# Performance work log

Hardware: AMD Instinct MI355X
Metric: run time of the kernel (lower is better)

Reference implementation:

```python
import jax, jax.numpy as jnp
import numpy as np

NX, NY = 256, 256            # img_size
NUM_DET, VIEW = 368, 180
SDD, SCD = 1000.0, 500.0
DCD = SDD - SCD
DET_INT = 2.0
PX = 1.0                     # pixel_size
SHIFT = 0.0                  # no quarter offset


def _geometry():
    # Faithful numpy port of FP.param_setting (equally_spaced mode)
    d_beta = np.pi * 360.0 / VIEW / 180.0
    beta = np.linspace(0.0, (VIEW - 1) * d_beta, VIEW)
    axis_x = np.linspace(-NX / 2, NX / 2, NX + 1) * PX          # [NX+1]
    axis_y = np.linspace(-NY / 2, NY / 2, NY + 1) * PX          # [NY+1]
    range_det_x = np.ones(NUM_DET) * DCD
    range_det_y = np.linspace(-(NUM_DET - 1) / 2, (NUM_DET - 1) / 2, NUM_DET) * DET_INT + SHIFT
    src = np.array([-SCD, 0.0])
    cb, sb = np.cos(beta), np.sin(beta)
    src_point = np.stack([src[0] * cb + src[1] * sb, -src[0] * sb + src[1] * cb])  # [2, V]
    det_x_rot = cb[None, :] * range_det_x[:, None] + sb[None, :] * range_det_y[:, None]   # [D, V]
    det_y_rot = -sb[None, :] * range_det_x[:, None] + cb[None, :] * range_det_y[:, None]  # [D, V]
    ax = (axis_x[:, None] - src_point[0][None, :])[None, :, :] / (det_x_rot - src_point[0])[:, None, :]  # [D, NX+1, V]
    ay = (axis_y[:, None] - src_point[1][None, :])[None, :, :] / (det_y_rot - src_point[1])[:, None, :]  # [D, NY+1, V]
    a_min = np.maximum(np.minimum(ax[:, 0, :], ax[:, -1, :]), np.minimum(ay[:, 0, :], ay[:, -1, :]))
    a_min[a_min < 0] = 0.0
    a_max = np.minimum(np.maximum(ax[:, 0, :], ax[:, -1, :]), np.maximum(ay[:, 0, :], ay[:, -1, :]))
    a_max[a_max > 1] = 1.0
    axy = np.concatenate([ax, ay], axis=1)                       # [D, NX+NY+2, V]
    axy[(axy > a_max[:, None, :]) | (axy < a_min[:, None, :])] = np.nan
    axy = np.sort(axy, axis=1)                                   # NaNs sort to the end (matches torch)
    diff_axy = np.diff(axy, n=1, axis=1)                         # [D, S, V], S = NX+NY+1
    a_mid = axy[:, :-1, :] + diff_axy / 2
    diff_axy = np.nan_to_num(diff_axy, nan=0.0)
    a_mid = np.nan_to_num(a_mid, nan=0.0)
    s2d = np.sqrt((det_x_rot - src_point[0]) ** 2 + (det_y_rot - src_point[1]) ** 2)  # [D, V]
    weighting = diff_axy.transpose(0, 2, 1)[None, None] * s2d[None, None, :, :, None]  # [1,1,D,V,S]
    x_pos = a_mid * (det_x_rot[:, None, :] - src_point[0]) + src_point[0]
    x_pos = x_pos.transpose(0, 2, 1) / (PX * (NX - 1) / 2)       # [D, V, S]
    y_pos = a_mid * (det_y_rot[:, None, :] - src_point[1]) + src_point[1]
    y_pos = y_pos.transpose(0, 2, 1) / (PX * (NY - 1) / 2)
    grid_pos = np.stack([x_pos, y_pos], axis=-1)                 # [D, V, S, 2]
    return grid_pos.astype(np.float32), weighting.astype(np.float32)


def _bilinear_sample(img, gx, gy):
    # torch.nn.functional.grid_sample: bilinear, padding_mode='zeros', align_corners=False
    # img: [B,C,H,W]; gx indexes W, gy indexes H; gx/gy: [D,V,S]
    B, C, H, W = img.shape
    ix = ((gx + 1.0) * W - 1.0) * 0.5
    iy = ((gy + 1.0) * H - 1.0) * 0.5
    ix0 = jnp.floor(ix)
    iy0 = jnp.floor(iy)
    wx1 = ix - ix0
    wy1 = iy - iy0
    out = jnp.zeros((B, C) + gx.shape, dtype=img.dtype)
    for dx in (0, 1):
        for dy in (0, 1):
            xi = ix0 + dx
            yi = iy0 + dy
            w = (wx1 if dx else 1.0 - wx1) * (wy1 if dy else 1.0 - wy1)
            valid = (xi >= 0) & (xi < W) & (yi >= 0) & (yi < H)
            xi_c = jnp.clip(xi, 0, W - 1).astype(jnp.int32)
            yi_c = jnp.clip(yi, 0, H - 1).astype(jnp.int32)
            out = out + img[:, :, yi_c, xi_c] * (w * valid)[None, None]
    return out  # [B,C,D,V,S]


def setup_inputs() -> dict:
    key = jax.random.key(0)
    img = jax.random.normal(key, (1, 1, NX, NY), dtype=jnp.float32)
    gp, wt = _geometry()
    return {"img": img, "grid_pos": jnp.asarray(gp), "weighting": jnp.asarray(wt)}


def reference(img, grid_pos, weighting):
    # All views vectorized at once (torch version loops over views)
    interp = _bilinear_sample(img, grid_pos[..., 0], grid_pos[..., 1])  # [B,C,D,V,S]
    sino = jnp.sum(weighting * interp, axis=-1)                         # [B,C,D,V]
    return jnp.where(jnp.isnan(sino), jnp.zeros((), sino.dtype), sino)
```

## Files before the change

### kernel.cpp

```cpp
#include <hip/hip_runtime.h>
#include <math.h>


constexpr int IMG_N  = 256;
constexpr int NDET   = 368;
constexpr int NVIEW  = 180;
constexpr int NSAMP  = 2 * IMG_N + 1;
constexpr int DV     = NDET * NVIEW;
constexpr int NITER  = (NSAMP + 63) / 64;

constexpr size_t PACK_BYTES = (size_t)IMG_N * IMG_N * sizeof(float4);
constexpr size_t RT_OFF     = PACK_BYTES;
constexpr size_t RT_BYTES   = (size_t)DV * 4 * sizeof(float4);
constexpr size_t KR_OFF     = RT_OFF + RT_BYTES;
constexpr size_t KR_BYTES   = (size_t)DV * sizeof(int4);
constexpr size_t WS_NEEDED  = KR_OFF + KR_BYTES;

__device__ __forceinline__ double valAP(double A, double s, double inv, int k) {
    return (A + s * (double)k) * inv;
}

__global__ __launch_bounds__(256) void pack_kernel(
    const float* __restrict__ img, float4* __restrict__ P)
{
    const int idx = blockIdx.x * 256 + threadIdx.x;
    const int y  = idx >> 8;
    const int x  = idx & 255;
    const int x1 = min(x + 1, IMG_N - 1);
    const int y1 = min(y + 1, IMG_N - 1);
    P[idx] = make_float4(img[y * IMG_N + x],  img[y * IMG_N + x1],
                         img[y1 * IMG_N + x], img[y1 * IMG_N + x1]);
}

__global__ __launch_bounds__(256) void geom_kernel(
    float4* __restrict__ rt, int4* __restrict__ kr)
{
    const int idx = blockIdx.x * 256 + threadIdx.x;
    if (idx >= DV) return;
    const int d = idx / NVIEW;
    const int v = idx - d * NVIEW;

    const double d_beta = ((M_PI * 360.0) / (double)NVIEW) / 180.0;
    const double stop   = (double)(NVIEW - 1) * d_beta;
    const double step   = stop / (double)(NVIEW - 1);
    const double beta   = (v == NVIEW - 1) ? stop : (double)v * step;
    const double cb = cos(beta), sb = sin(beta);

    const double sx  = -500.0 * cb;
    const double sy  =  500.0 * sb;
    const double rdy = ((double)d - 183.5) * 2.0;
    const double dx  = cb * 500.0 + sb * rdy;
    const double dy  = (-sb) * 500.0 + cb * rdy;
    const double ddx = dx - sx, ddy = dy - sy;

    double Ax, sxn;
    const double invx = 1.0 / ddx;
    if (invx >= 0.0) { Ax = -128.0 - sx; sxn = 1.0; }
    else             { Ax =  128.0 - sx; sxn = -1.0; }
    double Ay, syn;
    const double invy = 1.0 / ddy;
    if (invy >= 0.0) { Ay = -128.0 - sy; syn = 1.0; }
    else             { Ay =  128.0 - sy; syn = -1.0; }

    const double vx0 = valAP(Ax, sxn, invx, 0), vxN = valAP(Ax, sxn, invx, IMG_N);
    const double vy0 = valAP(Ay, syn, invy, 0), vyN = valAP(Ay, syn, invy, IMG_N);
    double a_min = fmax(vx0, vy0); if (a_min < 0.0) a_min = 0.0;
    double a_max = fmin(vxN, vyN); if (a_max > 1.0) a_max = 1.0;

    const double absdx = fabs(ddx), absdy = fabs(ddy);

    int klox, khix, kloy, khiy;
    {
        double kd = (a_min - vx0) * absdx;
        kd = fmin(fmax(kd, -1.0), 258.0);
        int k = (int)kd; k = max(0, min(k, 256));
        while (k > 0    && valAP(Ax, sxn, invx, k - 1) >= a_min) --k;
        while (k <= 256 && valAP(Ax, sxn, invx, k) < a_min)      ++k;
        klox = k;
        kd = (a_max - vx0) * absdx;
        kd = fmin(fmax(kd, -1.0), 258.0);
        k = (int)kd; k = max(0, min(k, 256));
        while (k > 0    && valAP(Ax, sxn, invx, k - 1) > a_max)  --k;
        while (k <= 256 && valAP(Ax, sxn, invx, k) <= a_max)     ++k;
        khix = k - 1;
        if (klox > khix) { klox = 0; khix = -1; }
    }
    {
        double kd = (a_min - vy0) * absdy;
        kd = fmin(fmax(kd, -1.0), 258.0);
        int k = (int)kd; k = max(0, min(k, 256));
        while (k > 0    && valAP(Ay, syn, invy, k - 1) >= a_min) --k;
        while (k <= 256 && valAP(Ay, syn, invy, k) < a_min)      ++k;
        kloy = k;
        kd = (a_max - vy0) * absdy;
        kd = fmin(fmax(kd, -1.0), 258.0);
        k = (int)kd; k = max(0, min(k, 256));
        while (k > 0    && valAP(Ay, syn, invy, k - 1) > a_max)  --k;
        while (k <= 256 && valAP(Ay, syn, invy, k) <= a_max)     ++k;
        khiy = k - 1;
        if (kloy > khiy) { kloy = 0; khiy = -1; }
    }

    const double s2d = sqrt(ddx * ddx + ddy * ddy);

    float4* o = rt + (size_t)idx * 4;
    o[0] = make_float4((float)(Ax * invx), (float)(sxn * invx),
                       (float)(Ay * invy), (float)(syn * invy));
    o[1] = make_float4((float)a_min, (float)((a_max - a_min) / 64.0),
                       (float)absdx, (float)absdy);
    o[2] = make_float4((float)(ddx * (128.0 / 127.5)),
                       (float)(sx  * (128.0 / 127.5) + 127.5),
                       (float)(ddy * (128.0 / 127.5)),
                       (float)(sy  * (128.0 / 127.5) + 127.5));
    o[3] = make_float4((float)s2d, 0.0f, 0.0f, 0.0f);
    kr[idx] = make_int4(klox, khix, kloy, khiy);
}

__device__ __forceinline__ int lbf(float t, float base, float step, float absd,
                                   int klo, int khi) {
    float kd = (t - fmaf((float)klo, step, base)) * absd + (float)klo;
    kd = fminf(fmaxf(kd, (float)klo - 1.0f), (float)khi + 2.0f);
    int k = (int)kd;
    k = max(klo, min(k, khi + 1));
    while (k > klo  && fmaf((float)(k - 1), step, base) >= t) --k;
    while (k <= khi && fmaf((float)k, step, base) < t)        ++k;
    return k;
}

__global__ __launch_bounds__(256) void fp_siddon(
    const float4* __restrict__ P,
    const float4* __restrict__ rt,
    const int4*   __restrict__ kr,
    float*        __restrict__ out)
{
    const int wave = threadIdx.x >> 6;
    const int lane = threadIdx.x & 63;
    const int dv   = __builtin_amdgcn_readfirstlane(blockIdx.x * 4 + wave);

    const float4 A = rt[(size_t)dv * 4 + 0];
    const float4 B = rt[(size_t)dv * 4 + 1];
    const float4 C = rt[(size_t)dv * 4 + 2];
    const float4 D = rt[(size_t)dv * 4 + 3];
    const int4 kk = kr[dv];

    float acc = 0.0f;
    const int M = (kk.y - kk.x + 1) + (kk.w - kk.z + 1);

    if (M >= 2) {
        const float HUGEF = 3e38f;
        const float tL = fmaf((float)lane, B.y, B.x);
        const float tH = (lane == 63) ? HUGEF : fmaf((float)(lane + 1), B.y, B.x);

        int kxb = (lane == 0) ? kk.x : lbf(tL, A.x, A.y, B.z, kk.x, kk.y);
        const int kxe = lbf(tH, A.x, A.y, B.z, kk.x, kk.y);
        int kyb = (lane == 0) ? kk.z : lbf(tL, A.z, A.w, B.w, kk.z, kk.w);
        const int kye = lbf(tH, A.z, A.w, B.w, kk.z, kk.w);

        const bool hpx = (kxb > kk.x), hpy = (kyb > kk.z);
        const float px = hpx ? fmaf((float)(kxb - 1), A.y, A.x) : -HUGEF;
        const float py = hpy ? fmaf((float)(kyb - 1), A.w, A.z) : -HUGEF;
        float prev = fmaxf(px, py);
        const bool hasp = hpx || hpy;

        int cnt = (kxe - kxb) + (kye - kyb);
        float vx = (kxb < kxe) ? fmaf((float)kxb, A.y, A.x) : HUGEF;
        float vy = (kyb < kye) ? fmaf((float)kyb, A.w, A.z) : HUGEF;

        if (!hasp && cnt > 0) {
            const bool tx = (vx <= vy);
            prev = tx ? vx : vy;
            if (tx) { ++kxb; vx = (kxb < kxe) ? fmaf((float)kxb, A.y, A.x) : HUGEF; }
            else    { ++kyb; vy = (kyb < kye) ? fmaf((float)kyb, A.w, A.z) : HUGEF; }
            --cnt;
        }

        while (cnt > 0) {
            const bool tx = (vx <= vy);
            const float cur = tx ? vx : vy;
            if (tx) { ++kxb; vx = (kxb < kxe) ? fmaf((float)kxb, A.y, A.x) : HUGEF; }
            else    { ++kyb; vy = (kyb < kye) ? fmaf((float)kyb, A.w, A.z) : HUGEF; }

            const float diff = cur - prev;
            const float mid  = fmaf(diff, 0.5f, prev);
            const float ix   = fmaf(mid, C.x, C.y);
            const float iy   = fmaf(mid, C.z, C.w);
            const float wf   = diff * D.x;

            const float fx0 = floorf(ix), fy0 = floorf(iy);
            const float wx1 = ix - fx0,  wy1 = iy - fy0;
            const int x0 = (int)fx0, y0 = (int)fy0;
            const int xc = min(max(x0, 0), IMG_N - 1);
            const int yb = min(max(y0, 0), IMG_N - 1);
            const float4 p = P[yb * IMG_N + xc];
            const bool loX = (x0 == -1), loY = (y0 == -1);
            const float a  = p.x;
            const float b2 = loX ? p.x : p.y;
            const float d2 = loX ? p.z : p.w;
            const float c3 = loY ? a  : p.z;
            const float d3 = loY ? b2 : d2;
            const float x0v = (((unsigned)x0)       < 256u) ? 1.0f : 0.0f;
            const float x1v = (((unsigned)(x0 + 1)) < 256u) ? 1.0f : 0.0f;
            const float my0 = (((unsigned)y0)       < 256u) ? 1.0f : 0.0f;
            const float my1 = (((unsigned)(y0 + 1)) < 256u) ? 1.0f : 0.0f;
            const float wx0 = 1.0f - wx1;
            const float wy0 = (1.0f - wy1) * my0;
            const float wy1m = wy1 * my1;
            const float interp = (a * x0v * wx0 + b2 * x1v * wx1) * wy0
                               + (c3 * x0v * wx0 + d3 * x1v * wx1) * wy1m;

            acc = fmaf(wf, interp, acc);
            prev = cur;
            --cnt;
        }
    }

    #pragma unroll
    for (int off = 32; off > 0; off >>= 1)
        acc += __shfl_down(acc, off, 64);
    if (lane == 0)
        out[dv] = isnan(acc) ? 0.0f : acc;
}

__global__ __launch_bounds__(256) void fp_kernel_nopack(
    const float*  __restrict__ img,
    const float2* __restrict__ grid,
    const float*  __restrict__ wt,
    float*        __restrict__ out)
{
    const int wave = threadIdx.x >> 6;
    const int lane = threadIdx.x & 63;
    const int dv   = blockIdx.x * 4 + wave;
    const long base = (long)dv * NSAMP;

    float2 g[NITER];
    float  w[NITER];
    #pragma unroll
    for (int k = 0; k < NITER; ++k) {
        const int s = lane + k * 64;
        if (s < NSAMP) { g[k] = grid[base + s]; w[k] = wt[base + s]; }
        else           { g[k] = make_float2(0.0f, 0.0f); w[k] = 0.0f; }
    }
    float acc = 0.0f;
    #pragma unroll
    for (int k = 0; k < NITER; ++k) {
        const float ix = ((g[k].x + 1.0f) * 256.0f - 1.0f) * 0.5f;
        const float iy = ((g[k].y + 1.0f) * 256.0f - 1.0f) * 0.5f;
        const float fx0 = floorf(ix), fy0 = floorf(iy);
        const float wx1 = ix - fx0,  wy1 = iy - fy0;
        const int x0 = (int)fx0, y0 = (int)fy0;
        const int xc  = min(max(x0, 0), IMG_N - 2);
        const int yc0 = min(max(y0, 0), IMG_N - 1);
        const int yc1 = min(max(y0 + 1, 0), IMG_N - 1);
        const float2 p0 = *(const float2*)(img + yc0 * IMG_N + xc);
        const float2 p1 = *(const float2*)(img + yc1 * IMG_N + xc);
        const bool x0v = ((unsigned)x0) < 256u;
        const bool x1v = ((unsigned)(x0 + 1)) < 256u;
        const bool hiX = (x0 == IMG_N - 1);
        const bool loX = (x0 == -1);
        const float v00 = x0v ? (hiX ? p0.y : p0.x) : 0.0f;
        const float v01 = x1v ? (loX ? p0.x : p0.y) : 0.0f;
        const float v10 = x0v ? (hiX ? p1.y : p1.x) : 0.0f;
        const float v11 = x1v ? (loX ? p1.x : p1.y) : 0.0f;
        const float my0 = (((unsigned)y0) < 256u) ? 1.0f : 0.0f;
        const float my1 = (((unsigned)(y0 + 1)) < 256u) ? 1.0f : 0.0f;
        const float wx0 = 1.0f - wx1;
        const float wy0 = (1.0f - wy1) * my0;
        const float wy1m = wy1 * my1;
        acc += w[k] * ((v00 * wx0 + v01 * wx1) * wy0
                     + (v10 * wx0 + v11 * wx1) * wy1m);
    }
    #pragma unroll
    for (int off = 32; off > 0; off >>= 1)
        acc += __shfl_down(acc, off, 64);
    if (lane == 0) out[dv] = isnan(acc) ? 0.0f : acc;
}

extern "C" void kernel_launch(void* const* d_in, const int* in_sizes, int n_in,
                              void* d_out, int out_size, void* d_ws, size_t ws_size,
                              hipStream_t stream) {
    const float*  img  = (const float*)d_in[0];
    const float2* grid = (const float2*)d_in[1];
    const float*  wt   = (const float*)d_in[2];
    float*        out  = (float*)d_out;

    if (ws_size >= WS_NEEDED) {
        float4* P  = (float4*)d_ws;
        float4* rt = (float4*)((char*)d_ws + RT_OFF);
        int4*   kr = (int4*)  ((char*)d_ws + KR_OFF);
        pack_kernel<<<IMG_N * IMG_N / 256, 256, 0, stream>>>(img, P);
        geom_kernel<<<(DV + 255) / 256, 256, 0, stream>>>(rt, kr);
        fp_siddon<<<DV / 4, 256, 0, stream>>>(P, rt, kr, out);
    } else {
        fp_kernel_nopack<<<DV / 4, 256, 0, stream>>>(img, grid, wt, out);
    }
}
```

Measured before the change: 436.5 us.

## Index merged Siddon crossings per lane and pack image corners as fp16

Replaces the per-lane segment walk (binary-search bounds then serial merge of x/y crossings) with a direct computation: each lane finds its q-th merged crossing through a linear estimate plus local correction, and takes the previous boundary from the neighbouring lane by shuffle. Work is spread evenly in chunks of 64 pairs, which removes the divergent variable-length loop. Separately, the packed corner image is stored as half2 pairs, halving gather bandwidth but adding fp16 rounding error to the pixel values. The per-ray geometry record shrinks from four float4 to three, and the index ranges become counts.

```diff
diff --git a/kernel.cpp b/kernel.cpp
--- a/kernel.cpp
+++ b/kernel.cpp
@@ -1,4 +1,5 @@
 #include <hip/hip_runtime.h>
+#include <hip/hip_fp16.h>
 #include <math.h>
 
 
@@ -9,11 +10,13 @@
 constexpr int DV     = NDET * NVIEW;
 constexpr int NITER  = (NSAMP + 63) / 64;
 
-constexpr size_t PACK_BYTES = (size_t)IMG_N * IMG_N * sizeof(float4);
+struct __align__(8) Corner { __half2 ab; __half2 cd; };
+
+constexpr size_t PACK_BYTES = (size_t)IMG_N * IMG_N * sizeof(Corner);
 constexpr size_t RT_OFF     = PACK_BYTES;
-constexpr size_t RT_BYTES   = (size_t)DV * 4 * sizeof(float4);
+constexpr size_t RT_BYTES   = (size_t)DV * 3 * sizeof(float4);
 constexpr size_t KR_OFF     = RT_OFF + RT_BYTES;
-constexpr size_t KR_BYTES   = (size_t)DV * sizeof(int4);
+constexpr size_t KR_BYTES   = (size_t)DV * sizeof(int2);
 constexpr size_t WS_NEEDED  = KR_OFF + KR_BYTES;
 
 __device__ __forceinline__ double valAP(double A, double s, double inv, int k) {
@@ -21,19 +24,21 @@
 }
 
 __global__ __launch_bounds__(256) void pack_kernel(
-    const float* __restrict__ img, float4* __restrict__ P)
+    const float* __restrict__ img, Corner* __restrict__ P)
 {
     const int idx = blockIdx.x * 256 + threadIdx.x;
     const int y  = idx >> 8;
     const int x  = idx & 255;
     const int x1 = min(x + 1, IMG_N - 1);
     const int y1 = min(y + 1, IMG_N - 1);
-    P[idx] = make_float4(img[y * IMG_N + x],  img[y * IMG_N + x1],
-                         img[y1 * IMG_N + x], img[y1 * IMG_N + x1]);
+    Corner c;
+    c.ab = __floats2half2_rn(img[y * IMG_N + x],  img[y * IMG_N + x1]);
+    c.cd = __floats2half2_rn(img[y1 * IMG_N + x], img[y1 * IMG_N + x1]);
+    P[idx] = c;
 }
 
 __global__ __launch_bounds__(256) void geom_kernel(
-    float4* __restrict__ rt, int4* __restrict__ kr)
+    float4* __restrict__ rt, int2* __restrict__ kr)
 {
     const int idx = blockIdx.x * 256 + threadIdx.x;
     if (idx >= DV) return;
@@ -101,117 +106,117 @@
         if (kloy > khiy) { kloy = 0; khiy = -1; }
     }
 
+    const int nx = khix - klox + 1;
+    const int ny = khiy - kloy + 1;
     const double s2d = sqrt(ddx * ddx + ddy * ddy);
 
-    float4* o = rt + (size_t)idx * 4;
-    o[0] = make_float4((float)(Ax * invx), (float)(sxn * invx),
-                       (float)(Ay * invy), (float)(syn * invy));
-    o[1] = make_float4((float)a_min, (float)((a_max - a_min) / 64.0),
-                       (float)absdx, (float)absdy);
+    const double sxd = sxn * invx, syd = syn * invy;
+    const double bxd = (Ax + sxn * (double)klox) * invx;
+    const double byd = (Ay + syn * (double)kloy) * invy;
+    const double ssum = sxd + syd;
+    const double c0 = (byd - bxd) / ssum;
+    const double c1 = syd / ssum;
+
+    float4* o = rt + (size_t)idx * 3;
+    o[0] = make_float4((float)bxd, (float)sxd, (float)byd, (float)syd);
+    o[1] = make_float4((float)c0, (float)c1, (float)s2d, 0.0f);
     o[2] = make_float4((float)(ddx * (128.0 / 127.5)),
                        (float)(sx  * (128.0 / 127.5) + 127.5),
                        (float)(ddy * (128.0 / 127.5)),
                        (float)(sy  * (128.0 / 127.5) + 127.5));
-    o[3] = make_float4((float)s2d, 0.0f, 0.0f, 0.0f);
-    kr[idx] = make_int4(klox, khix, kloy, khiy);
-}
-
-__device__ __forceinline__ int lbf(float t, float base, float step, float absd,
-                                   int klo, int khi) {
-    float kd = (t - fmaf((float)klo, step, base)) * absd + (float)klo;
-    kd = fminf(fmaxf(kd, (float)klo - 1.0f), (float)khi + 2.0f);
-    int k = (int)kd;
-    k = max(klo, min(k, khi + 1));
-    while (k > klo  && fmaf((float)(k - 1), step, base) >= t) --k;
-    while (k <= khi && fmaf((float)k, step, base) < t)        ++k;
-    return k;
+    kr[idx] = make_int2(nx, ny);
+}
+
+__device__ __forceinline__ float mergedq(int q, float bx, float sx, float by,
+                                         float sy, float c0, float c1,
+                                         int nx, int ny)
+{
+    const int t   = q + 1;
+    const int mlo = max(0, t - ny);
+    const int mhi = min(nx, t);
+    int m = (int)fmaf((float)q, c1, c0);
+    m = max(mlo, min(m, mhi));
+    while (m > mlo) {
+        const int mm = m - 1;
+        const bool Pmm = (t - 1 - mm < 0) || (mm >= nx) ||
+            (fmaf((float)(t - 1 - mm), sy, by) <= fmaf((float)mm, sx, bx));
+        if (!Pmm) break;
+        m = mm;
+    }
+    while (m < mhi) {
+        const bool Pm = (t - 1 - m < 0) || (m >= nx) ||
+            (fmaf((float)(t - 1 - m), sy, by) <= fmaf((float)m, sx, bx));
+        if (Pm) break;
+        ++m;
+    }
+    const float xl = (m > 0)     ? fmaf((float)(m - 1),     sx, bx) : -3e38f;
+    const float yl = (t - m > 0) ? fmaf((float)(t - 1 - m), sy, by) : -3e38f;
+    return fmaxf(xl, yl);
 }
 
 __global__ __launch_bounds__(256) void fp_siddon(
-    const float4* __restrict__ P,
+    const Corner* __restrict__ P,
     const float4* __restrict__ rt,
-    const int4*   __restrict__ kr,
+    const int2*   __restrict__ kr,
     float*        __restrict__ out)
 {
     const int wave = threadIdx.x >> 6;
     const int lane = threadIdx.x & 63;
     const int dv   = __builtin_amdgcn_readfirstlane(blockIdx.x * 4 + wave);
 
-    const float4 A = rt[(size_t)dv * 4 + 0];
-    const float4 B = rt[(size_t)dv * 4 + 1];
-    const float4 C = rt[(size_t)dv * 4 + 2];
-    const float4 D = rt[(size_t)dv * 4 + 3];
-    const int4 kk = kr[dv];
+    const float4 A = rt[(size_t)dv * 3 + 0];
+    const float4 B = rt[(size_t)dv * 3 + 1];
+    const float4 C = rt[(size_t)dv * 3 + 2];
+    const int2 nn = kr[dv];
+    const int nx = nn.x, ny = nn.y;
+    const int M = nx + ny;
+    const int npairs = M - 1;
 
     float acc = 0.0f;
-    const int M = (kk.y - kk.x + 1) + (kk.w - kk.z + 1);
-
-    if (M >= 2) {
-        const float HUGEF = 3e38f;
-        const float tL = fmaf((float)lane, B.y, B.x);
-        const float tH = (lane == 63) ? HUGEF : fmaf((float)(lane + 1), B.y, B.x);
-
-        int kxb = (lane == 0) ? kk.x : lbf(tL, A.x, A.y, B.z, kk.x, kk.y);
-        const int kxe = lbf(tH, A.x, A.y, B.z, kk.x, kk.y);
-        int kyb = (lane == 0) ? kk.z : lbf(tL, A.z, A.w, B.w, kk.z, kk.w);
-        const int kye = lbf(tH, A.z, A.w, B.w, kk.z, kk.w);
-
-        const bool hpx = (kxb > kk.x), hpy = (kyb > kk.z);
-        const float px = hpx ? fmaf((float)(kxb - 1), A.y, A.x) : -HUGEF;
-        const float py = hpy ? fmaf((float)(kyb - 1), A.w, A.z) : -HUGEF;
-        float prev = fmaxf(px, py);
-        const bool hasp = hpx || hpy;
-
-        int cnt = (kxe - kxb) + (kye - kyb);
-        float vx = (kxb < kxe) ? fmaf((float)kxb, A.y, A.x) : HUGEF;
-        float vy = (kyb < kye) ? fmaf((float)kyb, A.w, A.z) : HUGEF;
-
-        if (!hasp && cnt > 0) {
-            const bool tx = (vx <= vy);
-            prev = tx ? vx : vy;
-            if (tx) { ++kxb; vx = (kxb < kxe) ? fmaf((float)kxb, A.y, A.x) : HUGEF; }
-            else    { ++kyb; vy = (kyb < kye) ? fmaf((float)kyb, A.w, A.z) : HUGEF; }
-            --cnt;
-        }
-
-        while (cnt > 0) {
-            const bool tx = (vx <= vy);
-            const float cur = tx ? vx : vy;
-            if (tx) { ++kxb; vx = (kxb < kxe) ? fmaf((float)kxb, A.y, A.x) : HUGEF; }
-            else    { ++kyb; vy = (kyb < kye) ? fmaf((float)kyb, A.w, A.z) : HUGEF; }
-
-            const float diff = cur - prev;
-            const float mid  = fmaf(diff, 0.5f, prev);
-            const float ix   = fmaf(mid, C.x, C.y);
-            const float iy   = fmaf(mid, C.z, C.w);
-            const float wf   = diff * D.x;
-
-            const float fx0 = floorf(ix), fy0 = floorf(iy);
-            const float wx1 = ix - fx0,  wy1 = iy - fy0;
-            const int x0 = (int)fx0, y0 = (int)fy0;
-            const int xc = min(max(x0, 0), IMG_N - 1);
-            const int yb = min(max(y0, 0), IMG_N - 1);
-            const float4 p = P[yb * IMG_N + xc];
-            const bool loX = (x0 == -1), loY = (y0 == -1);
-            const float a  = p.x;
-            const float b2 = loX ? p.x : p.y;
-            const float d2 = loX ? p.z : p.w;
-            const float c3 = loY ? a  : p.z;
-            const float d3 = loY ? b2 : d2;
-            const float x0v = (((unsigned)x0)       < 256u) ? 1.0f : 0.0f;
-            const float x1v = (((unsigned)(x0 + 1)) < 256u) ? 1.0f : 0.0f;
-            const float my0 = (((unsigned)y0)       < 256u) ? 1.0f : 0.0f;
-            const float my1 = (((unsigned)(y0 + 1)) < 256u) ? 1.0f : 0.0f;
-            const float wx0 = 1.0f - wx1;
-            const float wy0 = (1.0f - wy1) * my0;
-            const float wy1m = wy1 * my1;
-            const float interp = (a * x0v * wx0 + b2 * x1v * wx1) * wy0
-                               + (c3 * x0v * wx0 + d3 * x1v * wx1) * wy1m;
-
-            acc = fmaf(wf, interp, acc);
-            prev = cur;
-            --cnt;
-        }
+
+    for (int base = 0; base < npairs; base += 64) {
+        const int p = base + lane;
+        const bool act = (p < npairs);
+        const int q = act ? p + 1 : 1;
+
+        const float cur = mergedq(q, A.x, A.y, A.z, A.w, B.x, B.y, nx, ny);
+        float prev = __shfl_up(cur, 1, 64);
+        if (lane == 0)
+            prev = mergedq(base, A.x, A.y, A.z, A.w, B.x, B.y, nx, ny);
+
+        const float diff = cur - prev;
+        const float mid  = fmaf(diff, 0.5f, prev);
+        const float ixp  = fmaf(mid, C.x, C.y);
+        const float iyp  = fmaf(mid, C.z, C.w);
+        const float wf   = act ? diff * B.z : 0.0f;
+
+        const float fx0 = floorf(ixp), fy0 = floorf(iyp);
+        const float wx1 = ixp - fx0,  wy1 = iyp - fy0;
+        const int x0 = (int)fx0, y0 = (int)fy0;
+        const int xc = min(max(x0, 0), IMG_N - 1);
+        const int yb = min(max(y0, 0), IMG_N - 1);
+
+        const Corner pc = P[yb * IMG_N + xc];
+        const float2 r0 = __half22float2(pc.ab);
+        const float2 r1 = __half22float2(pc.cd);
+
+        const bool loX = (x0 == -1), loY = (y0 == -1);
+        const float a  = r0.x;
+        const float b2 = loX ? r0.x : r0.y;
+        const float d2 = loX ? r1.x : r1.y;
+        const float c3 = loY ? a  : r1.x;
+        const float d3 = loY ? b2 : d2;
+        const float x0v = (((unsigned)x0)       < 256u) ? 1.0f : 0.0f;
+        const float x1v = (((unsigned)(x0 + 1)) < 256u) ? 1.0f : 0.0f;
+        const float my0 = (((unsigned)y0)       < 256u) ? 1.0f : 0.0f;
+        const float my1 = (((unsigned)(y0 + 1)) < 256u) ? 1.0f : 0.0f;
+        const float wx0 = 1.0f - wx1;
+        const float wy0 = (1.0f - wy1) * my0;
+        const float wy1m = wy1 * my1;
+        const float interp = (a * x0v * wx0 + b2 * x1v * wx1) * wy0
+                           + (c3 * x0v * wx0 + d3 * x1v * wx1) * wy1m;
+
+        acc = fmaf(wf, interp, acc);
     }
 
     #pragma unroll
@@ -284,9 +289,9 @@
     float*        out  = (float*)d_out;
 
     if (ws_size >= WS_NEEDED) {
-        float4* P  = (float4*)d_ws;
+        Corner* P  = (Corner*)d_ws;
         float4* rt = (float4*)((char*)d_ws + RT_OFF);
-        int4*   kr = (int4*)  ((char*)d_ws + KR_OFF);
+        int2*   kr = (int2*)  ((char*)d_ws + KR_OFF);
         pack_kernel<<<IMG_N * IMG_N / 256, 256, 0, stream>>>(img, P);
         geom_kernel<<<(DV + 255) / 256, 256, 0, stream>>>(rt, kr);
         fp_siddon<<<DV / 4, 256, 0, stream>>>(P, rt, kr, out);
```

Result: faster. 413.3 us (-5.3%).
